# Optimization experiments

Hardware: AMD Instinct MI355X
Metric: run time of the kernel (lower is better)

## Reference

```python
import jax, jax.numpy as jnp
import numpy as np

B, H = 16384, 1024
EPS = 1e-5


def setup_inputs() -> dict:
    key = jax.random.key(0)
    ks = jax.random.split(key, 12)
    inp = {
        "t": 0,
        "h": jax.random.normal(ks[0], (B, H), jnp.float32),
        "e": jax.random.normal(ks[1], (B, H), jnp.float32),
        # LiquidNeuron params
        "W_rec": jax.random.normal(ks[2], (H, H), jnp.float32) * 0.1,
        "bias": jnp.zeros((H,), jnp.float32),
        "tau": jnp.ones((H,), jnp.float32),
        "decay": jnp.ones((H,), jnp.float32),
        "ln_w": jnp.ones((H,), jnp.float32),
        "ln_b": jnp.zeros((H,), jnp.float32),
        # context_encoder: Linear -> ReLU -> Linear (dropout = identity in eval)
        "ce_w1": jax.random.normal(ks[3], (H, H), jnp.float32) * (1.0 / np.sqrt(H)),
        "ce_b1": jnp.zeros((H,), jnp.float32),
        "ce_w2": jax.random.normal(ks[4], (H, H), jnp.float32) * (1.0 / np.sqrt(H)),
        "ce_b2": jnp.zeros((H,), jnp.float32),
        # param_modulator
        "pm_w": jax.random.normal(ks[5], (H, H), jnp.float32) * (1.0 / np.sqrt(H)),
        "pm_b": jnp.zeros((H,), jnp.float32),
    }
    return inp


def reference(t, h, e, W_rec, bias, tau, decay, ln_w, ln_b,
              ce_w1, ce_b1, ce_w2, ce_b2, pm_w, pm_b):
    # context encoder (eval mode: dropout is identity)
    context = jnp.maximum(h @ ce_w1.T + ce_b1, 0.0) @ ce_w2.T + ce_b2  # [B,H]
    pa = context @ pm_w.T + pm_b  # param_adjustment [B,H]
    # bmm(e[:,None,:], (W_rec*(1+pa)[:,:,None]).T) == (1+pa) * (e @ W_rec.T)
    matmul_result = (1.0 + pa) * (e @ W_rec.T)  # [B,H]
    tau_adjusted = tau * jax.nn.sigmoid(pa)  # [B,H]
    dh_dt = (-decay * h + matmul_result + bias) / tau_adjusted
    # LayerNorm over last dim
    mu = jnp.mean(dh_dt, axis=-1, keepdims=True)
    var = jnp.var(dh_dt, axis=-1, keepdims=True)
    dh_dt = (dh_dt - mu) * jax.lax.rsqrt(var + EPS) * ln_w + ln_b
    return dh_dt
```

## Files before the change

### kernel.cpp

```cpp
#include <hip/hip_runtime.h>
#include <stdint.h>

#define H_DIM 1024
#define B_DIM 16384

typedef unsigned short u16;
typedef short bf16x8 __attribute__((ext_vector_type(8)));
typedef unsigned short ushort8 __attribute__((ext_vector_type(8)));
typedef float f32x4 __attribute__((ext_vector_type(4)));

__device__ __forceinline__ u16 f2bf(float f) {
  union { float f; uint32_t u; } v; v.f = f;
  uint32_t r = v.u + 0x7fffu + ((v.u >> 16) & 1u);
  return (u16)(r >> 16);
}
__device__ __forceinline__ float bf2f(u16 x) {
  union { uint32_t u; float f; } v; v.u = ((uint32_t)x) << 16;
  return v.f;
}
__device__ __forceinline__ ushort4 cvt4(float4 a) {
  ushort4 o;
  o.x = f2bf(a.x); o.y = f2bf(a.y); o.z = f2bf(a.z); o.w = f2bf(a.w);
  return o;
}

#define GLDS16(gsrc, ldst)                                                                 \
  __builtin_amdgcn_global_load_lds((const __attribute__((address_space(1))) void*)(gsrc),  \
                                   (__attribute__((address_space(3))) void*)(ldst), 16, 0, 0)

__global__ __launch_bounds__(256) void cvt_all(const float* __restrict__ h,
                                               const float* __restrict__ e,
                                               const float* __restrict__ w1f,
                                               const float* __restrict__ pmwf,
                                               const float* __restrict__ wrecf,
                                               u16* __restrict__ hb, u16* __restrict__ eb,
                                               u16* __restrict__ o1, u16* __restrict__ o3,
                                               u16* __restrict__ o4,
                                               const float* __restrict__ tau,
                                               float* __restrict__ rtau) {
  const int b = blockIdx.x;
  const int t = threadIdx.x;
  const float* in;
  u16* out;
  int chunk;
  if (b < 2048) {
    in = h; out = hb; chunk = b;
  } else if (b < 4096) {
    in = e; out = eb; chunk = b - 2048;
  } else if (b < 4224) {
    in = w1f; out = o1; chunk = b - 4096;
  } else if (b < 4352) {
    in = pmwf; out = o3; chunk = b - 4224;
  } else if (b < 4480) {
    in = wrecf; out = o4; chunk = b - 4352;
  } else {
    for (int i = t; i < H_DIM; i += 256) rtau[i] = 1.0f / tau[i];
    return;
  }
  const float4* in4 = (const float4*)in + (size_t)chunk * 2048 + t;
  ushort4* out4 = (ushort4*)out + (size_t)chunk * 2048 + t;
  float4 v[8];
#pragma unroll
  for (int k = 0; k < 8; ++k) v[k] = in4[k * 256];
#pragma unroll
  for (int k = 0; k < 8; ++k) out4[k * 256] = cvt4(v[k]);
}

__global__ __launch_bounds__(256) void tr_cvt_w2_b32(const float* __restrict__ in,
                                                     u16* __restrict__ out,
                                                     const float* __restrict__ pmw,
                                                     const float* __restrict__ ceb2,
                                                     const float* __restrict__ pmb,
                                                     float* __restrict__ b32) {
  const int t = threadIdx.x;
  if (blockIdx.x >= 256) {
    const int i = (blockIdx.x - 256) * 256 + t;
    const float4* w4 = (const float4*)(pmw + (size_t)i * H_DIM);
    const float4* b4 = (const float4*)ceb2;
    float acc = pmb[i];
    for (int k = 0; k < 256; ++k) {
      float4 w = w4[k], b = b4[k];
      acc += w.x * b.x + w.y * b.y + w.z * b.z + w.w * b.w;
    }
    b32[i] = acc;
    return;
  }
  __shared__ float tile[64][65];
  const int r0 = (blockIdx.x >> 4) * 64;
  const int c0 = (blockIdx.x & 15) * 64;
  const float4* in4 = (const float4*)in;
#pragma unroll
  for (int it = 0; it < 4; ++it) {
    const int idx = it * 256 + t;
    const int r = idx >> 4, c4 = idx & 15;
    float4 v = in4[(size_t)(r0 + r) * 256 + (c0 >> 2) + c4];
    tile[r][c4 * 4 + 0] = v.x; tile[r][c4 * 4 + 1] = v.y;
    tile[r][c4 * 4 + 2] = v.z; tile[r][c4 * 4 + 3] = v.w;
  }
  __syncthreads();
  ushort4* out4 = (ushort4*)out;
#pragma unroll
  for (int it = 0; it < 4; ++it) {
    const int idx = it * 256 + t;
    const int c = idx >> 4, r4 = idx & 15;
    ushort4 o;
    o.x = f2bf(tile[r4 * 4 + 0][c]); o.y = f2bf(tile[r4 * 4 + 1][c]);
    o.z = f2bf(tile[r4 * 4 + 2][c]); o.w = f2bf(tile[r4 * 4 + 3][c]);
    out4[(size_t)(c0 + c) * 256 + (r0 >> 2) + r4] = o;
  }
}

__global__ __launch_bounds__(256) void w32_gemm(const u16* __restrict__ A,
                                                const u16* __restrict__ Wt,
                                                u16* __restrict__ C) {
  const int t = threadIdx.x;
  const int wv = t >> 6, l = t & 63;
  const int l15 = l & 15, lg = l >> 4;
  const int m0 = (blockIdx.x >> 4) * 64 + (wv >> 1) * 32;
  const int n0 = (blockIdx.x & 15) * 64 + (wv & 1) * 32;

  const u16* ap0 = A + (size_t)(m0 + l15) * H_DIM + lg * 8;
  const u16* ap1 = ap0 + 16 * H_DIM;
  const u16* bp0 = Wt + (size_t)(n0 + l15) * H_DIM + lg * 8;
  const u16* bp1 = bp0 + 16 * H_DIM;

  f32x4 acc[2][2] = {};
#pragma unroll
  for (int kt = 0; kt < 32; ++kt) {
    bf16x8 aF[2], bF[2];
    aF[0] = *(const bf16x8*)(ap0 + kt * 32);
    aF[1] = *(const bf16x8*)(ap1 + kt * 32);
    bF[0] = *(const bf16x8*)(bp0 + kt * 32);
    bF[1] = *(const bf16x8*)(bp1 + kt * 32);
#pragma unroll
    for (int mi = 0; mi < 2; ++mi)
#pragma unroll
      for (int ni = 0; ni < 2; ++ni)
        acc[mi][ni] =
            __builtin_amdgcn_mfma_f32_16x16x32_bf16(aF[mi], bF[ni], acc[mi][ni], 0, 0, 0);
  }
#pragma unroll
  for (int mi = 0; mi < 2; ++mi)
#pragma unroll
    for (int ni = 0; ni < 2; ++ni) {
      const int col = n0 + ni * 16 + l15;
#pragma unroll
      for (int j = 0; j < 4; ++j) {
        const int row = m0 + mi * 16 + lg * 4 + j;
        C[(size_t)row * H_DIM + col] = f2bf(acc[mi][ni][j]);
      }
    }
}

template <int MODE>
__device__ __forceinline__ void subtile_step(u16* shp, int slot, int slot3, int aoff, int boff,
                                             int wv, const u16*& pA0, const u16*& pA1,
                                             const u16*& pB0, const u16*& pB1,
                                             f32x4 (&acc)[8][4]) {
  const u16* Ab = shp + slot * 16384 + aoff;
  const u16* Bb = shp + slot * 16384 + 8192 + boff;
  bf16x8 aF[8], bF[4];
#pragma unroll
  for (int i = 0; i < 4; ++i) aF[i] = *(const bf16x8*)(Ab + i * 512);
#pragma unroll
  for (int i = 0; i < 4; ++i) bF[i] = *(const bf16x8*)(Bb + i * 512);
#pragma unroll
  for (int i = 4; i < 8; ++i) aF[i] = *(const bf16x8*)(Ab + i * 512);
  if (MODE == 3) {
    u16* da = shp + slot3 * 16384 + wv * 1024;
    GLDS16(pA0, da); GLDS16(pA1, da + 512);
    u16* db = shp + slot3 * 16384 + 8192 + wv * 1024;
    GLDS16(pB0, db); GLDS16(pB1, db + 512);
    pA0 += 32; pA1 += 32; pB0 += 32; pB1 += 32;
  }
  __builtin_amdgcn_s_setprio(1);
#pragma unroll
  for (int mf = 0; mf < 8; ++mf)
#pragma unroll
    for (int nf = 0; nf < 4; ++nf)
      acc[mf][nf] = __builtin_amdgcn_mfma_f32_16x16x32_bf16(aF[mf], bF[nf], acc[mf][nf], 0, 0, 0);
  __builtin_amdgcn_s_setprio(0);
  if (MODE == 3) asm volatile("s_waitcnt vmcnt(8)" ::: "memory");
  if (MODE == 2) asm volatile("s_waitcnt vmcnt(4)" ::: "memory");
  if (MODE == 1) asm volatile("s_waitcnt vmcnt(0)" ::: "memory");
  __builtin_amdgcn_s_barrier();
}

template <bool RELU, bool HASBIAS, typename OUT>
__global__ __launch_bounds__(512, 2) void gemm256(const u16* __restrict__ A,
                                                  const u16* __restrict__ W,
                                                  const float* __restrict__ bias,
                                                  OUT* __restrict__ C) {
  extern __shared__ u16 sh[];
  const int t = threadIdx.x;
  const int wv = t >> 6, l = t & 63;
  const int wm = wv >> 2, wn = wv & 3;
  const int l15 = l & 15, lg = l >> 4;

  const int bid = blockIdx.x;
  const int logical = (bid & 7) * 32 + (bid >> 3);
  const int m0 = (logical >> 2) * 256;
  const int n0 = (logical & 3) * 256;

  const int koff = (lg ^ ((l15 >> 1) & 3)) * 8;
  const int aoff = (wm * 128 + l15) * 32 + koff;
  const int boff = (wn * 64 + l15) * 32 + koff;

  const int rowst = wv * 32 + (l >> 2);
  const int ksl = ((l & 3) ^ ((l >> 3) & 3)) * 8;
  const u16* pA0 = A + (size_t)(m0 + rowst) * H_DIM + ksl;
  const u16* pA1 = pA0 + 16 * H_DIM;
  const u16* pB0 = W + (size_t)(n0 + rowst) * H_DIM + ksl;
  const u16* pB1 = pB0 + 16 * H_DIM;

  f32x4 acc[8][4] = {};

#pragma unroll
  for (int s = 0; s < 3; ++s) {
    u16* da = sh + s * 16384 + wv * 1024;
    GLDS16(pA0, da); GLDS16(pA1, da + 512);
    u16* db = sh + s * 16384 + 8192 + wv * 1024;
    GLDS16(pB0, db); GLDS16(pB1, db + 512);
    pA0 += 32; pA1 += 32; pB0 += 32; pB1 += 32;
  }
  asm volatile("s_waitcnt vmcnt(8)" ::: "memory");
  __builtin_amdgcn_s_barrier();

  for (int s = 0; s < 29; ++s)
    subtile_step<3>(sh, s & 3, (s + 3) & 3, aoff, boff, wv, pA0, pA1, pB0, pB1, acc);
  subtile_step<2>(sh, 1, 0, aoff, boff, wv, pA0, pA1, pB0, pB1, acc);
  subtile_step<1>(sh, 2, 0, aoff, boff, wv, pA0, pA1, pB0, pB1, acc);
  subtile_step<0>(sh, 3, 0, aoff, boff, wv, pA0, pA1, pB0, pB1, acc);

  float bv[4];
#pragma unroll
  for (int nf = 0; nf < 4; ++nf)
    bv[nf] = HASBIAS ? bias[n0 + wn * 64 + nf * 16 + l15] : 0.0f;
#pragma unroll
  for (int mf = 0; mf < 8; ++mf) {
#pragma unroll
    for (int nf = 0; nf < 4; ++nf) {
      const int col = n0 + wn * 64 + nf * 16 + l15;
#pragma unroll
      for (int j = 0; j < 4; ++j) {
        const int row = m0 + wm * 128 + mf * 16 + lg * 4 + j;
        float v = acc[mf][nf][j] + bv[nf];
        if (RELU) v = fmaxf(v, 0.0f);
        if constexpr (sizeof(OUT) == 2)
          C[(size_t)row * H_DIM + col] = (OUT)f2bf(v);
        else
          C[(size_t)row * H_DIM + col] = v;
      }
    }
  }
}

__global__ __launch_bounds__(256) void liquid_ln(const u16* __restrict__ hb,
                                                 const u16* __restrict__ pa,
                                                 const u16* __restrict__ ev,
                                                 const float* __restrict__ bias,
                                                 const float* __restrict__ rtau,
                                                 const float* __restrict__ decay,
                                                 const float* __restrict__ lnw,
                                                 const float* __restrict__ lnb,
                                                 float* __restrict__ out) {
  const int wv = threadIdx.x >> 6, l = threadIdx.x & 63;
  const int row = blockIdx.x * 4 + wv;
  const size_t rb = (size_t)row * H_DIM;

  float d[16];
  float s = 0.f, ss = 0.f;
#pragma unroll
  for (int c = 0; c < 2; ++c) {
    const int col = c * 512 + l * 8;
    float b8[8], r8[8], dc8[8];
    *(float4*)b8 = *(const float4*)(bias + col);
    *(float4*)(b8 + 4) = *(const float4*)(bias + col + 4);
    *(float4*)r8 = *(const float4*)(rtau + col);
    *(float4*)(r8 + 4) = *(const float4*)(rtau + col + 4);
    *(float4*)dc8 = *(const float4*)(decay + col);
    *(float4*)(dc8 + 4) = *(const float4*)(decay + col + 4);
    ushort8 hv = *(const ushort8*)(hb + rb + col);
    ushort8 pv = *(const ushort8*)(pa + rb + col);
    ushort8 evv = *(const ushort8*)(ev + rb + col);
#pragma unroll
    for (int j = 0; j < 8; ++j) {
      const float hf = bf2f(hv[j]);
      const float p = bf2f(pv[j]);
      const float e = bf2f(evv[j]);
      const float num = fmaf(-dc8[j], hf, fmaf(1.0f + p, e, b8[j]));
      const float val = num * (1.0f + __expf(-p)) * r8[j];
      d[c * 8 + j] = val;
      s += val;
      ss += val * val;
    }
  }
#pragma unroll
  for (int off = 32; off; off >>= 1) {
    s += __shfl_xor(s, off);
    ss += __shfl_xor(ss, off);
  }
  const float mu = s * (1.0f / H_DIM);
  const float var = ss * (1.0f / H_DIM) - mu * mu;
  const float rstd = rsqrtf(var + 1e-5f);

#pragma unroll
  for (int c = 0; c < 2; ++c) {
    const int col = c * 512 + l * 8;
    float w8[8], lb8[8], o[8];
    *(float4*)w8 = *(const float4*)(lnw + col);
    *(float4*)(w8 + 4) = *(const float4*)(lnw + col + 4);
    *(float4*)lb8 = *(const float4*)(lnb + col);
    *(float4*)(lb8 + 4) = *(const float4*)(lnb + col + 4);
#pragma unroll
    for (int j = 0; j < 8; ++j) o[j] = fmaf((d[c * 8 + j] - mu) * rstd, w8[j], lb8[j]);
    *(float4*)(out + rb + col) = *(float4*)o;
    *(float4*)(out + rb + col + 4) = *(float4*)(o + 4);
  }
}

extern "C" void kernel_launch(void* const* d_in, const int* in_sizes, int n_in,
                              void* d_out, int out_size, void* d_ws, size_t ws_size,
                              hipStream_t stream) {
  const float* h = (const float*)d_in[1];
  const float* e = (const float*)d_in[2];
  const float* Wrec = (const float*)d_in[3];
  const float* bias = (const float*)d_in[4];
  const float* tau = (const float*)d_in[5];
  const float* decay = (const float*)d_in[6];
  const float* lnw = (const float*)d_in[7];
  const float* lnb = (const float*)d_in[8];
  const float* ce_w1 = (const float*)d_in[9];
  const float* ce_b1 = (const float*)d_in[10];
  const float* ce_w2 = (const float*)d_in[11];
  const float* ce_b2 = (const float*)d_in[12];
  const float* pm_w = (const float*)d_in[13];
  const float* pm_b = (const float*)d_in[14];
  float* out = (float*)d_out;

  char* ws = (char*)d_ws;
  const size_t MB = 1024 * 1024;
  u16* w1b = (u16*)(ws + 0 * MB);
  u16* w2t = (u16*)(ws + 2 * MB);
  u16* w3b = (u16*)(ws + 4 * MB);
  u16* w4b = (u16*)(ws + 6 * MB);
  u16* W32b = (u16*)(ws + 8 * MB);
  float* rtau = (float*)(ws + 10 * MB);
  float* b32 = (float*)(ws + 10 * MB + 8192);
  u16* hbf = (u16*)(ws + 12 * MB);
  u16* ebf = (u16*)(ws + 44 * MB);
  u16* t1 = (u16*)(ws + 76 * MB);
  u16* evb = (u16*)(ws + 76 * MB);
  u16* pab = (u16*)(ws + 108 * MB);

  cvt_all<<<4481, 256, 0, stream>>>(h, e, ce_w1, pm_w, Wrec, hbf, ebf, w1b, w3b, w4b, tau, rtau);
  tr_cvt_w2_b32<<<260, 256, 0, stream>>>(ce_w2, w2t, pm_w, ce_b2, pm_b, b32);
  w32_gemm<<<256, 256, 0, stream>>>(w3b, w2t, W32b);

  const int LDS_BYTES = 131072;
  hipFuncSetAttribute((const void*)gemm256<true, true, u16>,
                      hipFuncAttributeMaxDynamicSharedMemorySize, LDS_BYTES);
  hipFuncSetAttribute((const void*)gemm256<false, true, u16>,
                      hipFuncAttributeMaxDynamicSharedMemorySize, LDS_BYTES);
  hipFuncSetAttribute((const void*)gemm256<false, false, u16>,
                      hipFuncAttributeMaxDynamicSharedMemorySize, LDS_BYTES);

  const int NWG = (B_DIM / 256) * (H_DIM / 256);
  gemm256<true, true, u16><<<NWG, 512, LDS_BYTES, stream>>>(hbf, w1b, ce_b1, t1);
  gemm256<false, true, u16><<<NWG, 512, LDS_BYTES, stream>>>(t1, W32b, b32, pab);
  gemm256<false, false, u16><<<NWG, 512, LDS_BYTES, stream>>>(ebf, w4b, nullptr, evb);

  liquid_ln<<<B_DIM / 4, 256, 0, stream>>>(hbf, pab, evb, bias, rtau, decay, lnw, lnb, out);
}
```

Before: 218.9 us.

## Fuse w2 transpose kernel into cvt_all, widen stores, issue async loads earlier

Merges the w2 transpose/convert and the bias-fold blocks into the main conversion kernel, which removes one kernel launch. The conversion path now has each thread handle two consecutive float4 inputs and write a single 16-byte ushort8 instead of strided ushort4 stores. In the GEMM subtile step, the global-to-LDS prefetch is issued before the LDS fragment reads so it overlaps more of the step. The cost is extra static shared memory in every cvt_all block, which may reduce occupancy.

```diff
diff --git a/kernel.cpp b/kernel.cpp
--- a/kernel.cpp
+++ b/kernel.cpp
@@ -37,9 +37,57 @@
                                                u16* __restrict__ o1, u16* __restrict__ o3,
                                                u16* __restrict__ o4,
                                                const float* __restrict__ tau,
-                                               float* __restrict__ rtau) {
+                                               float* __restrict__ rtau,
+                                               const float* __restrict__ w2f,
+                                               u16* __restrict__ w2t,
+                                               const float* __restrict__ ceb2,
+                                               const float* __restrict__ pmb,
+                                               float* __restrict__ b32) {
+  __shared__ float tile[64][65];
   const int b = blockIdx.x;
   const int t = threadIdx.x;
+
+  if (b >= 4480) {
+    if (b < 4736) {
+      const int bb = b - 4480;
+      const int r0 = (bb >> 4) * 64;
+      const int c0 = (bb & 15) * 64;
+      const float4* in4 = (const float4*)w2f;
+#pragma unroll
+      for (int it = 0; it < 4; ++it) {
+        const int idx = it * 256 + t;
+        const int r = idx >> 4, c4 = idx & 15;
+        float4 v = in4[(size_t)(r0 + r) * 256 + (c0 >> 2) + c4];
+        tile[r][c4 * 4 + 0] = v.x; tile[r][c4 * 4 + 1] = v.y;
+        tile[r][c4 * 4 + 2] = v.z; tile[r][c4 * 4 + 3] = v.w;
+      }
+      __syncthreads();
+      ushort4* out4 = (ushort4*)w2t;
+#pragma unroll
+      for (int it = 0; it < 4; ++it) {
+        const int idx = it * 256 + t;
+        const int c = idx >> 4, r4 = idx & 15;
+        ushort4 o;
+        o.x = f2bf(tile[r4 * 4 + 0][c]); o.y = f2bf(tile[r4 * 4 + 1][c]);
+        o.z = f2bf(tile[r4 * 4 + 2][c]); o.w = f2bf(tile[r4 * 4 + 3][c]);
+        out4[(size_t)(c0 + c) * 256 + (r0 >> 2) + r4] = o;
+      }
+    } else if (b < 4740) {
+      const int i = (b - 4736) * 256 + t;
+      const float4* w4 = (const float4*)(pmwf + (size_t)i * H_DIM);
+      const float4* b4 = (const float4*)ceb2;
+      float acc = pmb[i];
+      for (int k = 0; k < 256; ++k) {
+        float4 w = w4[k], bb2 = b4[k];
+        acc += w.x * bb2.x + w.y * bb2.y + w.z * bb2.z + w.w * bb2.w;
+      }
+      b32[i] = acc;
+    } else {
+      for (int i = t; i < H_DIM; i += 256) rtau[i] = 1.0f / tau[i];
+    }
+    return;
+  }
+
   const float* in;
   u16* out;
   int chunk;
@@ -51,62 +99,26 @@
     in = w1f; out = o1; chunk = b - 4096;
   } else if (b < 4352) {
     in = pmwf; out = o3; chunk = b - 4224;
-  } else if (b < 4480) {
+  } else {
     in = wrecf; out = o4; chunk = b - 4352;
-  } else {
-    for (int i = t; i < H_DIM; i += 256) rtau[i] = 1.0f / tau[i];
-    return;
-  }
-  const float4* in4 = (const float4*)in + (size_t)chunk * 2048 + t;
-  ushort4* out4 = (ushort4*)out + (size_t)chunk * 2048 + t;
+  }
+  const float4* in4 = (const float4*)in + (size_t)chunk * 2048;
+  ushort8* out8 = (ushort8*)out + (size_t)chunk * 1024;
   float4 v[8];
 #pragma unroll
-  for (int k = 0; k < 8; ++k) v[k] = in4[k * 256];
-#pragma unroll
-  for (int k = 0; k < 8; ++k) out4[k * 256] = cvt4(v[k]);
-}
-
-__global__ __launch_bounds__(256) void tr_cvt_w2_b32(const float* __restrict__ in,
-                                                     u16* __restrict__ out,
-                                                     const float* __restrict__ pmw,
-                                                     const float* __restrict__ ceb2,
-                                                     const float* __restrict__ pmb,
-                                                     float* __restrict__ b32) {
-  const int t = threadIdx.x;
-  if (blockIdx.x >= 256) {
-    const int i = (blockIdx.x - 256) * 256 + t;
-    const float4* w4 = (const float4*)(pmw + (size_t)i * H_DIM);
-    const float4* b4 = (const float4*)ceb2;
-    float acc = pmb[i];
-    for (int k = 0; k < 256; ++k) {
-      float4 w = w4[k], b = b4[k];
-      acc += w.x * b.x + w.y * b.y + w.z * b.z + w.w * b.w;
-    }
-    b32[i] = acc;
-    return;
-  }
-  __shared__ float tile[64][65];
-  const int r0 = (blockIdx.x >> 4) * 64;
-  const int c0 = (blockIdx.x & 15) * 64;
-  const float4* in4 = (const float4*)in;
-#pragma unroll
-  for (int it = 0; it < 4; ++it) {
-    const int idx = it * 256 + t;
-    const int r = idx >> 4, c4 = idx & 15;
-    float4 v = in4[(size_t)(r0 + r) * 256 + (c0 >> 2) + c4];
-    tile[r][c4 * 4 + 0] = v.x; tile[r][c4 * 4 + 1] = v.y;
-    tile[r][c4 * 4 + 2] = v.z; tile[r][c4 * 4 + 3] = v.w;
-  }
-  __syncthreads();
-  ushort4* out4 = (ushort4*)out;
-#pragma unroll
-  for (int it = 0; it < 4; ++it) {
-    const int idx = it * 256 + t;
-    const int c = idx >> 4, r4 = idx & 15;
-    ushort4 o;
-    o.x = f2bf(tile[r4 * 4 + 0][c]); o.y = f2bf(tile[r4 * 4 + 1][c]);
-    o.z = f2bf(tile[r4 * 4 + 2][c]); o.w = f2bf(tile[r4 * 4 + 3][c]);
-    out4[(size_t)(c0 + c) * 256 + (r0 >> 2) + r4] = o;
+  for (int g = 0; g < 4; ++g) {
+    const int oi = g * 256 + t;
+    v[2 * g] = in4[2 * oi];
+    v[2 * g + 1] = in4[2 * oi + 1];
+  }
+#pragma unroll
+  for (int g = 0; g < 4; ++g) {
+    const int oi = g * 256 + t;
+    ushort4 lo = cvt4(v[2 * g]), hi = cvt4(v[2 * g + 1]);
+    ushort8 o;
+    o[0] = lo.x; o[1] = lo.y; o[2] = lo.z; o[3] = lo.w;
+    o[4] = hi.x; o[5] = hi.y; o[6] = hi.z; o[7] = hi.w;
+    out8[oi] = o;
   }
 }
 
@@ -157,15 +169,6 @@
                                              int wv, const u16*& pA0, const u16*& pA1,
                                              const u16*& pB0, const u16*& pB1,
                                              f32x4 (&acc)[8][4]) {
-  const u16* Ab = shp + slot * 16384 + aoff;
-  const u16* Bb = shp + slot * 16384 + 8192 + boff;
-  bf16x8 aF[8], bF[4];
-#pragma unroll
-  for (int i = 0; i < 4; ++i) aF[i] = *(const bf16x8*)(Ab + i * 512);
-#pragma unroll
-  for (int i = 0; i < 4; ++i) bF[i] = *(const bf16x8*)(Bb + i * 512);
-#pragma unroll
-  for (int i = 4; i < 8; ++i) aF[i] = *(const bf16x8*)(Ab + i * 512);
   if (MODE == 3) {
     u16* da = shp + slot3 * 16384 + wv * 1024;
     GLDS16(pA0, da); GLDS16(pA1, da + 512);
@@ -173,6 +176,15 @@
     GLDS16(pB0, db); GLDS16(pB1, db + 512);
     pA0 += 32; pA1 += 32; pB0 += 32; pB1 += 32;
   }
+  const u16* Ab = shp + slot * 16384 + aoff;
+  const u16* Bb = shp + slot * 16384 + 8192 + boff;
+  bf16x8 aF[8], bF[4];
+#pragma unroll
+  for (int i = 0; i < 4; ++i) aF[i] = *(const bf16x8*)(Ab + i * 512);
+#pragma unroll
+  for (int i = 0; i < 4; ++i) bF[i] = *(const bf16x8*)(Bb + i * 512);
+#pragma unroll
+  for (int i = 4; i < 8; ++i) aF[i] = *(const bf16x8*)(Ab + i * 512);
   __builtin_amdgcn_s_setprio(1);
 #pragma unroll
   for (int mf = 0; mf < 8; ++mf)
@@ -353,8 +365,8 @@
   u16* evb = (u16*)(ws + 76 * MB);
   u16* pab = (u16*)(ws + 108 * MB);
 
-  cvt_all<<<4481, 256, 0, stream>>>(h, e, ce_w1, pm_w, Wrec, hbf, ebf, w1b, w3b, w4b, tau, rtau);
-  tr_cvt_w2_b32<<<260, 256, 0, stream>>>(ce_w2, w2t, pm_w, ce_b2, pm_b, b32);
+  cvt_all<<<4741, 256, 0, stream>>>(h, e, ce_w1, pm_w, Wrec, hbf, ebf, w1b, w3b, w4b, tau, rtau,
+                                    ce_w2, w2t, ce_b2, pm_b, b32);
   w32_gemm<<<256, 256, 0, stream>>>(w3b, w2t, W32b);
 
   const int LDS_BYTES = 131072;
```

Result: no change. 215.1 us (-1.7%).
